# Optimization experiments

Measured on AMD Instinct MI355X. Metric: run time of the kernel, lower is better.

Reference implementation:

```python
import jax, jax.numpy as jnp
import numpy as np

# ---- CRF hyperparameters (init_kwargs) ----
NUM_CLASSES = 4
RADIUS = 10            # guided filter radius -> 21x21 kernel
EPS = 1e-4
THETA_GAMMA = 2.5
G_RADIUS = int(THETA_GAMMA * 4)  # gaussian layer radius = 10 -> 21x21 kernel
SPATIAL_COMPAT = 3.0
BILATERAL_COMPAT = 10.0
NUM_ITERATIONS = 5
RGB_W = np.array([0.2989, 0.5870, 0.1140], dtype=np.float32)  # tf rgb_to_grayscale


def _make_kernel(radius, theta):
    x, y = np.mgrid[-radius:radius + 1, -radius:radius + 1]
    k = np.exp(-(x ** 2 + y ** 2) / (2.0 * theta ** 2))
    k = k / k.sum()
    k[radius, radius] = 0.0  # zero out center (no self-message)
    return jnp.asarray(k, dtype=jnp.float32)

_GAUSS_K = _make_kernel(G_RADIUS, THETA_GAMMA)          # spatial gaussian kernel
_GUIDED_K = _make_kernel(RADIUS, RADIUS / 3.0)          # guided-filter gaussian kernel


def _depthwise(src, k2d, r):
    # src: [B,H,W,C], k2d: [kh,kw]; zero-padded depthwise conv (same as pad+VALID)
    c = src.shape[-1]
    kh, kw = k2d.shape
    k = jnp.broadcast_to(k2d[:, :, None, None], (kh, kw, 1, c))
    return jax.lax.conv_general_dilated(
        src, k, window_strides=(1, 1), padding=[(r, r), (r, r)],
        dimension_numbers=('NHWC', 'HWIO', 'NHWC'), feature_group_count=c)


def _gaussian(src):
    return _depthwise(src, _GAUSS_K, G_RADIUS)


def _guided(gray, p):
    # guided gaussian filter with single-channel guide `gray` [B,H,W,1]
    gf = lambda s: _depthwise(s, _GUIDED_K, RADIUS)
    mean_I = gf(gray)                       # [B,H,W,1]
    mean_p = gf(p)                          # [B,H,W,C]
    mean_Ip = gf(gray * p)
    cov_Ip = mean_Ip - mean_I * mean_p
    mean_II = gf(gray * gray)
    var_I = mean_II - mean_I * mean_I
    a = cov_Ip / (var_I + EPS)
    b = mean_p - a * mean_I
    return gf(a) * gray + gf(b)


def setup_inputs() -> dict:
    key = jax.random.key(0)
    k1, k2 = jax.random.split(key)
    unary = jax.random.normal(k1, (1, 512, 512, NUM_CLASSES), dtype=jnp.float32)
    image = jax.random.uniform(k2, (1, 512, 512, 3), dtype=jnp.float32)
    return {"unary": unary, "image": image}


def reference(unary, image):
    gray = (image @ jnp.asarray(RGB_W))[..., None]        # [B,H,W,1]
    ones = jnp.ones_like(unary)
    spatial_norm = _gaussian(ones)
    bilateral_norm = _guided(gray, ones)

    Q = jax.nn.softmax(-unary, axis=-1)
    for _ in range(NUM_ITERATIONS):
        spatial_out = _gaussian(Q) / spatial_norm
        bilateral_out = _guided(gray, Q) / bilateral_norm
        # spatial_weights = SPATIAL_COMPAT*I, bilateral_weights = BILATERAL_COMPAT*I,
        # compatibility = -I  => matmuls reduce to scalar scaling + negation
        message = SPATIAL_COMPAT * spatial_out + BILATERAL_COMPAT * bilateral_out
        pairwise = -message
        Q = jax.nn.softmax(-unary - pairwise, axis=-1)
    return Q
```

## Files before the change

kernel.cpp:

```cpp
#include <hip/hip_runtime.h>
#include <hip/hip_cooperative_groups.h>
#include <math.h>

namespace cg = cooperative_groups;

#define W 512
#define H 512
#define NPIX (W*H)
#define RAD 10
#define KS 21
#define CRF_EPS 1e-4f

#define TX 32
#define TY 8
#define CIN (TX + 2*RAD)
#define RIN (TY + 2*RAD)
#define GX (W / TX)
#define GY (H / TY)
#define NBLK (GX*GY)
#define NVT (CIN * 4)

#define SM_BYTES 29952
#define OFF_R1 23296

struct W21 { float w[KS]; };

struct Params {
    const float4* unary;
    const float*  image;
    float*  gray;
    float4* Q;
    float2* a1b1;
    float4* a_arr;
    float4* b_arr;
    float4* Qfinal;
    W21 wg, wu;
    float c0g, c0u;
};

__device__ __forceinline__ float4 f4(float x, float y, float z, float w_) {
    return make_float4(x, y, z, w_);
}
__device__ __forceinline__ float4 fma4(float s, float4 a, float4 acc) {
    acc.x = fmaf(s, a.x, acc.x); acc.y = fmaf(s, a.y, acc.y);
    acc.z = fmaf(s, a.z, acc.z); acc.w = fmaf(s, a.w, acc.w);
    return acc;
}
__device__ __forceinline__ int swz(int b, int N) {
    return (b & 7) * (N >> 3) + (b >> 3);
}


__global__ __launch_bounds__(256, 5) void k_crf(Params P) {
    cg::grid_group grid = cg::this_grid();
    __shared__ __align__(16) char smem[SM_BYTES];
    float4* sQ  = (float4*)smem;
    float2* s2t = (float2*)smem;
    float2* ii0 = (float2*)smem;
    float*  sG  = (float*)(smem + OFF_R1);
    float2* ii1 = (float2*)(smem + OFF_R1);
    float4* i0  = (float4*)smem;
    float4* i1  = (float4*)(smem + 6656);
    float4* i2  = (float4*)(smem + OFF_R1);
    float4* ia  = (float4*)(smem + OFF_R1);
    float4* ib  = (float4*)smem;

    int t = threadIdx.x;
    int L = swz(blockIdx.x, NBLK);
    int x0 = (L & (GX - 1)) * TX, y0 = (L >> 4) * TY;
    int row = t >> 5, col = t & 31;
    int py = y0 + row, px = x0 + col;
    int p = py * W + px;
    int vc = t % CIN, vr0 = (t / CIN) * 2;
    int cidx = (row + RAD) * CIN + col + RAD;

    {
        int pi = blockIdx.x * 256 + t;
        float r = P.image[3 * pi], g = P.image[3 * pi + 1], b = P.image[3 * pi + 2];
        P.gray[pi] = 0.2989f * r + 0.5870f * g + 0.1140f * b;
        float4 u0 = P.unary[pi];
        float mn = fminf(fminf(u0.x, u0.y), fminf(u0.z, u0.w));
        float ex = expf(mn - u0.x), ey = expf(mn - u0.y);
        float ez = expf(mn - u0.z), ew = expf(mn - u0.w);
        float inv = 1.f / (ex + ey + ez + ew);
        P.Q[pi] = f4(ex * inv, ey * inv, ez * inv, ew * inv);
    }
    float4 u = P.unary[p];
    float Sgx = 0.f, Sgy = 0.f, Sux = 0.f, Suy = 0.f;
    #pragma unroll
    for (int d = -RAD; d <= RAD; ++d) {
        int xx = px + d, yy = py + d;
        if (xx >= 0 && xx < W) { Sgx += P.wg.w[d + RAD]; Sux += P.wu.w[d + RAD]; }
        if (yy >= 0 && yy < H) { Sgy += P.wg.w[d + RAD]; Suy += P.wu.w[d + RAD]; }
    }
    float s3 = 3.f / (Sgx * Sgy - P.c0g);
    grid.sync();

    for (int i = t; i < RIN * CIN; i += 256) {
        int r = i / CIN, c = i - r * CIN;
        int gx = x0 + c - RAD, gy = y0 + r - RAD;
        float g = 0.f;
        if ((unsigned)gx < W && (unsigned)gy < H) g = P.gray[gy * W + gx];
        sG[i] = g;
    }
    __syncthreads();
    if (t < NVT) {
        float2 acc0 = make_float2(0.f, 0.f), acc1 = acc0;
        #pragma unroll
        for (int s = 0; s < 22; ++s) {
            float g = sG[(vr0 + s) * CIN + vc];
            if (s <= 20) { float wgv = P.wu.w[s] * g; acc0.x += wgv; acc0.y = fmaf(wgv, g, acc0.y); }
            if (s >= 1)  { float wgv = P.wu.w[s-1] * g; acc1.x += wgv; acc1.y = fmaf(wgv, g, acc1.y); }
        }
        ii0[vr0 * CIN + vc] = acc0;
        ii0[(vr0 + 1) * CIN + vc] = acc1;
    }
    __syncthreads();
    float gv = sG[cidx];
    float mI, iv, ibn;
    {
        float2 A = make_float2(0.f, 0.f);
        #pragma unroll
        for (int d = 0; d < KS; ++d) {
            float2 v = ii0[row * CIN + col + d];
            A.x = fmaf(P.wu.w[d], v.x, A.x);
            A.y = fmaf(P.wu.w[d], v.y, A.y);
        }
        mI = A.x - P.c0u * gv;
        float mII = A.y - P.c0u * gv * gv;
        iv = 1.f / ((mII - mI * mI) + CRF_EPS);
        float N = Sux * Suy - P.c0u;
        float a1v = mI * (1.f - N) * iv;
        float b1v = N - a1v * mI;
        P.a1b1[p] = make_float2(a1v, b1v);
    }
    grid.sync();

    for (int i = t; i < RIN * CIN; i += 256) {
        int r = i / CIN, c = i - r * CIN;
        int gx = x0 + c - RAD, gy = y0 + r - RAD;
        float2 v = make_float2(0.f, 0.f);
        if ((unsigned)gx < W && (unsigned)gy < H) v = P.a1b1[gy * W + gx];
        s2t[i] = v;
    }
    __syncthreads();
    if (t < NVT) {
        float2 acc0 = make_float2(0.f, 0.f), acc1 = acc0;
        #pragma unroll
        for (int s = 0; s < 22; ++s) {
            float2 v = s2t[(vr0 + s) * CIN + vc];
            if (s <= 20) { acc0.x = fmaf(P.wu.w[s], v.x, acc0.x); acc0.y = fmaf(P.wu.w[s], v.y, acc0.y); }
            if (s >= 1)  { acc1.x = fmaf(P.wu.w[s-1], v.x, acc1.x); acc1.y = fmaf(P.wu.w[s-1], v.y, acc1.y); }
        }
        ii1[vr0 * CIN + vc] = acc0;
        ii1[(vr0 + 1) * CIN + vc] = acc1;
    }
    __syncthreads();
    {
        float2 A = make_float2(0.f, 0.f);
        #pragma unroll
        for (int d = 0; d < KS; ++d) {
            float2 v = ii1[row * CIN + col + d];
            A.x = fmaf(P.wu.w[d], v.x, A.x);
            A.y = fmaf(P.wu.w[d], v.y, A.y);
        }
        float2 cen = s2t[cidx];
        float va = A.x - P.c0u * cen.x;
        float vb = A.y - P.c0u * cen.y;
        ibn = 10.f / (va * gv + vb);
    }

    float px_part, py_part, pz_part, pw_part;
    for (int it = 0; it < 5; ++it) {
        __syncthreads();
        for (int i = t; i < RIN * CIN; i += 256) {
            int r = i / CIN, c = i - r * CIN;
            int gx = x0 + c - RAD, gy = y0 + r - RAD;
            float4 q = f4(0.f, 0.f, 0.f, 0.f); float g = 0.f;
            if ((unsigned)gx < W && (unsigned)gy < H) {
                int pp = gy * W + gx; q = P.Q[pp]; g = P.gray[pp];
            }
            sQ[i] = q; sG[i] = g;
        }
        __syncthreads();
        float4 Qc = sQ[cidx];
        float4 a0[2], a1r[2], a2[2];
        if (t < NVT) {
            #pragma unroll
            for (int j = 0; j < 2; ++j) { a0[j] = f4(0,0,0,0); a1r[j] = a0[j]; a2[j] = a0[j]; }
            #pragma unroll
            for (int s = 0; s < 22; ++s) {
                float4 q = sQ[(vr0 + s) * CIN + vc];
                float g = sG[(vr0 + s) * CIN + vc];
                float4 gq = f4(g * q.x, g * q.y, g * q.z, g * q.w);
                if (s <= 20) {
                    a0[0]  = fma4(P.wg.w[s], q, a0[0]);
                    a1r[0] = fma4(P.wu.w[s], q, a1r[0]);
                    a2[0]  = fma4(P.wu.w[s], gq, a2[0]);
                }
                if (s >= 1) {
                    a0[1]  = fma4(P.wg.w[s-1], q, a0[1]);
                    a1r[1] = fma4(P.wu.w[s-1], q, a1r[1]);
                    a2[1]  = fma4(P.wu.w[s-1], gq, a2[1]);
                }
            }
        }
        __syncthreads();
        if (t < NVT) {
            #pragma unroll
            for (int j = 0; j < 2; ++j) {
                i0[(vr0 + j) * CIN + vc] = a0[j];
                i1[(vr0 + j) * CIN + vc] = a1r[j];
                i2[(vr0 + j) * CIN + vc] = a2[j];
            }
        }
        __syncthreads();
        {
            float4 A0 = f4(0,0,0,0), A1 = A0, A2 = A0;
            #pragma unroll
            for (int d = 0; d < KS; ++d) {
                A0 = fma4(P.wg.w[d], i0[row * CIN + col + d], A0);
                A1 = fma4(P.wu.w[d], i1[row * CIN + col + d], A1);
                A2 = fma4(P.wu.w[d], i2[row * CIN + col + d], A2);
            }
            float4 g4  = fma4(-P.c0g, Qc, A0);
            float4 m4  = fma4(-P.c0u, Qc, A1);
            float4 mi4 = fma4(-P.c0u * gv, Qc, A2);
            float4 a, b;
            a.x = (mi4.x - mI * m4.x) * iv; a.y = (mi4.y - mI * m4.y) * iv;
            a.z = (mi4.z - mI * m4.z) * iv; a.w = (mi4.w - mI * m4.w) * iv;
            b.x = m4.x - a.x * mI; b.y = m4.y - a.y * mI;
            b.z = m4.z - a.z * mI; b.w = m4.w - a.w * mI;
            px_part = fmaf(s3, g4.x, -u.x); py_part = fmaf(s3, g4.y, -u.y);
            pz_part = fmaf(s3, g4.z, -u.z); pw_part = fmaf(s3, g4.w, -u.w);
            P.a_arr[p] = a; P.b_arr[p] = b;
        }
        grid.sync();

        for (int i = t; i < RIN * CIN; i += 256) {
            int r = i / CIN, c = i - r * CIN;
            int gx = x0 + c - RAD, gy = y0 + r - RAD;
            float4 v = f4(0.f, 0.f, 0.f, 0.f);
            if ((unsigned)gx < W && (unsigned)gy < H) v = P.a_arr[gy * W + gx];
            sQ[i] = v;
        }
        __syncthreads();
        float4 Ac = sQ[cidx];
        if (t < NVT) {
            float4 va0 = f4(0,0,0,0), va1 = va0;
            #pragma unroll
            for (int s = 0; s < 22; ++s) {
                float4 v = sQ[(vr0 + s) * CIN + vc];
                if (s <= 20) va0 = fma4(P.wu.w[s], v, va0);
                if (s >= 1)  va1 = fma4(P.wu.w[s-1], v, va1);
            }
            ia[vr0 * CIN + vc] = va0;
            ia[(vr0 + 1) * CIN + vc] = va1;
        }
        __syncthreads();
        for (int i = t; i < RIN * CIN; i += 256) {
            int r = i / CIN, c = i - r * CIN;
            int gx = x0 + c - RAD, gy = y0 + r - RAD;
            float4 v = f4(0.f, 0.f, 0.f, 0.f);
            if ((unsigned)gx < W && (unsigned)gy < H) v = P.b_arr[gy * W + gx];
            sQ[i] = v;
        }
        __syncthreads();
        float4 Bc = sQ[cidx];
        float4 vb0 = f4(0,0,0,0), vb1 = vb0;
        if (t < NVT) {
            #pragma unroll
            for (int s = 0; s < 22; ++s) {
                float4 v = sQ[(vr0 + s) * CIN + vc];
                if (s <= 20) vb0 = fma4(P.wu.w[s], v, vb0);
                if (s >= 1)  vb1 = fma4(P.wu.w[s-1], v, vb1);
            }
        }
        __syncthreads();
        if (t < NVT) {
            ib[vr0 * CIN + vc] = vb0;
            ib[(vr0 + 1) * CIN + vc] = vb1;
        }
        __syncthreads();
        {
            float4 VA = f4(0,0,0,0), VB = VA;
            #pragma unroll
            for (int d = 0; d < KS; ++d) {
                VA = fma4(P.wu.w[d], ia[row * CIN + col + d], VA);
                VB = fma4(P.wu.w[d], ib[row * CIN + col + d], VB);
            }
            float4 a4 = fma4(-P.c0u, Ac, VA);
            float4 b4 = fma4(-P.c0u, Bc, VB);
            float lx = fmaf(fmaf(a4.x, gv, b4.x), ibn, px_part);
            float ly = fmaf(fmaf(a4.y, gv, b4.y), ibn, py_part);
            float lz = fmaf(fmaf(a4.z, gv, b4.z), ibn, pz_part);
            float lw = fmaf(fmaf(a4.w, gv, b4.w), ibn, pw_part);
            float m = fmaxf(fmaxf(lx, ly), fmaxf(lz, lw));
            float ex = expf(lx - m), ey = expf(ly - m);
            float ez = expf(lz - m), ew = expf(lw - m);
            float inv = 1.f / (ex + ey + ez + ew);
            float4 qn = f4(ex * inv, ey * inv, ez * inv, ew * inv);
            if (it == 4) P.Qfinal[p] = qn;
            else         P.Q[p] = qn;
        }
        if (it < 4) grid.sync();
    }
}


__global__ __launch_bounds__(256) void fb_init(const float* __restrict__ img,
        const float4* __restrict__ unary, float* __restrict__ gray,
        float4* __restrict__ Q, float* __restrict__ Sg, float* __restrict__ Su,
        W21 wg, W21 wu) {
    int t = threadIdx.x;
    if (blockIdx.x < 2) {
        int x = blockIdx.x * 256 + t;
        float sg = 0.f, su = 0.f;
        #pragma unroll
        for (int d = -RAD; d <= RAD; ++d) {
            int xx = x + d;
            if (xx >= 0 && xx < W) { sg += wg.w[d + RAD]; su += wu.w[d + RAD]; }
        }
        Sg[x] = sg; Su[x] = su;
    }
    int b = swz(blockIdx.x, NPIX / 256);
    int p = b * 256 + t;
    float r = img[3 * p], g = img[3 * p + 1], bch = img[3 * p + 2];
    gray[p] = 0.2989f * r + 0.5870f * g + 0.1140f * bch;
    float4 u = unary[p];
    float mn = fminf(fminf(u.x, u.y), fminf(u.z, u.w));
    float ex = expf(mn - u.x), ey = expf(mn - u.y), ez = expf(mn - u.z), ew = expf(mn - u.w);
    float inv = 1.f / (ex + ey + ez + ew);
    Q[p] = f4(ex * inv, ey * inv, ez * inv, ew * inv);
}

__global__ __launch_bounds__(256, 4) void fb_s1(const float* __restrict__ gray,
        const float* __restrict__ Su, float* __restrict__ mean_I,
        float* __restrict__ inv_var, float2* __restrict__ a1b1,
        W21 wu, float c0u) {
    __shared__ float  sg[RIN][CIN];
    __shared__ float2 ii[TY][CIN];
    int L = swz(blockIdx.x, NBLK);
    int x0 = (L & (GX - 1)) * TX, y0 = (L >> 4) * TY;
    int t = threadIdx.x;
    for (int i = t; i < RIN * CIN; i += 256) {
        int r = i / CIN, c = i - r * CIN;
        int gx = x0 + c - RAD, gy = y0 + r - RAD;
        float g = 0.f;
        if ((unsigned)gx < W && (unsigned)gy < H) g = gray[gy * W + gx];
        sg[r][c] = g;
    }
    __syncthreads();
    if (t < NVT) {
        int c = t % CIN, r0 = (t / CIN) * 2;
        float2 acc0 = make_float2(0.f, 0.f), acc1 = acc0;
        #pragma unroll
        for (int s = 0; s < 22; ++s) {
            float g = sg[r0 + s][c];
            if (s <= 20) { float wgv = wu.w[s] * g; acc0.x += wgv; acc0.y = fmaf(wgv, g, acc0.y); }
            if (s >= 1)  { float wgv = wu.w[s-1] * g; acc1.x += wgv; acc1.y = fmaf(wgv, g, acc1.y); }
        }
        ii[r0][c] = acc0; ii[r0 + 1][c] = acc1;
    }
    __syncthreads();
    int row = t >> 5, col = t & 31;
    float2 A = make_float2(0.f, 0.f);
    #pragma unroll
    for (int d = 0; d < KS; ++d) {
        float2 v = ii[row][col + d];
        A.x = fmaf(wu.w[d], v.x, A.x);
        A.y = fmaf(wu.w[d], v.y, A.y);
    }
    int py = y0 + row, px = x0 + col;
    int p = py * W + px;
    float gc = sg[row + RAD][col + RAD];
    float mI = A.x - c0u * gc;
    float mII = A.y - c0u * gc * gc;
    float iv = 1.f / ((mII - mI * mI) + CRF_EPS);
    float N = Su[px] * Su[py] - c0u;
    float av = mI * (1.f - N) * iv;
    float bv = N - av * mI;
    mean_I[p] = mI; inv_var[p] = iv; a1b1[p] = make_float2(av, bv);
}

__global__ __launch_bounds__(256, 4) void fb_s2(const float2* __restrict__ a1b1,
        const float* __restrict__ gray, float* __restrict__ inv_bn,
        W21 wu, float c0u) {
    __shared__ float2 s2[RIN][CIN];
    __shared__ float2 ii[TY][CIN];
    int L = swz(blockIdx.x, NBLK);
    int x0 = (L & (GX - 1)) * TX, y0 = (L >> 4) * TY;
    int t = threadIdx.x;
    for (int i = t; i < RIN * CIN; i += 256) {
        int r = i / CIN, c = i - r * CIN;
        int gx = x0 + c - RAD, gy = y0 + r - RAD;
        float2 v = make_float2(0.f, 0.f);
        if ((unsigned)gx < W && (unsigned)gy < H) v = a1b1[gy * W + gx];
        s2[r][c] = v;
    }
    __syncthreads();
    if (t < NVT) {
        int c = t % CIN, r0 = (t / CIN) * 2;
        float2 acc0 = make_float2(0.f, 0.f), acc1 = acc0;
        #pragma unroll
        for (int s = 0; s < 22; ++s) {
            float2 v = s2[r0 + s][c];
            if (s <= 20) { acc0.x = fmaf(wu.w[s], v.x, acc0.x); acc0.y = fmaf(wu.w[s], v.y, acc0.y); }
            if (s >= 1)  { acc1.x = fmaf(wu.w[s-1], v.x, acc1.x); acc1.y = fmaf(wu.w[s-1], v.y, acc1.y); }
        }
        ii[r0][c] = acc0; ii[r0 + 1][c] = acc1;
    }
    __syncthreads();
    int row = t >> 5, col = t & 31;
    float2 A = make_float2(0.f, 0.f);
    #pragma unroll
    for (int d = 0; d < KS; ++d) {
        float2 v = ii[row][col + d];
        A.x = fmaf(wu.w[d], v.x, A.x);
        A.y = fmaf(wu.w[d], v.y, A.y);
    }
    int p = (y0 + row) * W + x0 + col;
    float2 cen = s2[row + RAD][col + RAD];
    float va = A.x - c0u * cen.x;
    float vb = A.y - c0u * cen.y;
    inv_bn[p] = 1.f / (va * gray[p] + vb);
}

__global__ __launch_bounds__(256, 4) void fb_f1(const float4* __restrict__ Q,
        const float* __restrict__ gray, const float* __restrict__ mean_I,
        const float* __restrict__ inv_var, const float* __restrict__ Sg,
        const float4* __restrict__ unary, float4* __restrict__ a_out,
        float4* __restrict__ b_out, float4* __restrict__ partial,
        W21 wg, W21 wu, float c0g, float c0u) {
    __shared__ __align__(16) char smem[23296 + 5824 + 6656];
    float4* sQ = (float4*)smem;
    float*  sG = (float*)(smem + 23296);
    float4* i2 = (float4*)(smem + 23296 + 5824);
    float4* i0 = (float4*)smem;
    float4* i1 = (float4*)(smem + 6656);
    int L = swz(blockIdx.x, NBLK);
    int x0 = (L & (GX - 1)) * TX, y0 = (L >> 4) * TY;
    int t = threadIdx.x;
    for (int i = t; i < RIN * CIN; i += 256) {
        int r = i / CIN, c = i - r * CIN;
        int gx = x0 + c - RAD, gy = y0 + r - RAD;
        float4 q = f4(0.f, 0.f, 0.f, 0.f); float g = 0.f;
        if ((unsigned)gx < W && (unsigned)gy < H) {
            int p = gy * W + gx; q = Q[p]; g = gray[p];
        }
        sQ[i] = q; sG[i] = g;
    }
    __syncthreads();
    int row = t >> 5, col = t & 31;
    int py = y0 + row, px = x0 + col;
    int p = py * W + px;
    float mI = mean_I[p], iv = inv_var[p];
    float4 u = unary[p];
    float sgx = Sg[px], sgy = Sg[py];
    float4 Qc = sQ[(row + RAD) * CIN + col + RAD];
    float  gc = sG[(row + RAD) * CIN + col + RAD];
    float4 a0[2], a1[2], a2[2];
    int vc = t % CIN, vr0 = (t / CIN) * 2;
    if (t < NVT) {
        #pragma unroll
        for (int j = 0; j < 2; ++j) { a0[j] = f4(0,0,0,0); a1[j] = a0[j]; a2[j] = a0[j]; }
        #pragma unroll
        for (int s = 0; s < 22; ++s) {
            float4 q = sQ[(vr0 + s) * CIN + vc];
            float g = sG[(vr0 + s) * CIN + vc];
            float4 gq = f4(g * q.x, g * q.y, g * q.z, g * q.w);
            if (s <= 20) {
                a0[0] = fma4(wg.w[s], q, a0[0]);
                a1[0] = fma4(wu.w[s], q, a1[0]);
                a2[0] = fma4(wu.w[s], gq, a2[0]);
            }
            if (s >= 1) {
                a0[1] = fma4(wg.w[s-1], q, a0[1]);
                a1[1] = fma4(wu.w[s-1], q, a1[1]);
                a2[1] = fma4(wu.w[s-1], gq, a2[1]);
            }
        }
    }
    __syncthreads();
    if (t < NVT) {
        #pragma unroll
        for (int j = 0; j < 2; ++j) {
            i0[(vr0 + j) * CIN + vc] = a0[j];
            i1[(vr0 + j) * CIN + vc] = a1[j];
            i2[(vr0 + j) * CIN + vc] = a2[j];
        }
    }
    __syncthreads();
    float4 A0 = f4(0,0,0,0), A1 = A0, A2 = A0;
    #pragma unroll
    for (int d = 0; d < KS; ++d) {
        A0 = fma4(wg.w[d], i0[row * CIN + col + d], A0);
        A1 = fma4(wu.w[d], i1[row * CIN + col + d], A1);
        A2 = fma4(wu.w[d], i2[row * CIN + col + d], A2);
    }
    float4 g4  = fma4(-c0g, Qc, A0);
    float4 m4  = fma4(-c0u, Qc, A1);
    float4 mi4 = fma4(-c0u * gc, Qc, A2);
    float4 a, b;
    a.x = (mi4.x - mI * m4.x) * iv; a.y = (mi4.y - mI * m4.y) * iv;
    a.z = (mi4.z - mI * m4.z) * iv; a.w = (mi4.w - mI * m4.w) * iv;
    b.x = m4.x - a.x * mI; b.y = m4.y - a.y * mI;
    b.z = m4.z - a.z * mI; b.w = m4.w - a.w * mI;
    float s3 = 3.f / (sgx * sgy - c0g);
    float4 part = f4(fmaf(s3, g4.x, -u.x), fmaf(s3, g4.y, -u.y),
                     fmaf(s3, g4.z, -u.z), fmaf(s3, g4.w, -u.w));
    a_out[p] = a; b_out[p] = b; partial[p] = part;
}

__global__ __launch_bounds__(256, 4) void fb_f2(const float4* __restrict__ A,
        const float4* __restrict__ B, const float4* __restrict__ partial,
        const float* __restrict__ gray, const float* __restrict__ inv_bn,
        float4* __restrict__ Qout, W21 wu, float c0u) {
    __shared__ __align__(16) char smem[23296 + 6656];
    float4* sT = (float4*)smem;
    float4* ia = (float4*)(smem + 23296);
    float4* ib = (float4*)smem;
    int L = swz(blockIdx.x, NBLK);
    int x0 = (L & (GX - 1)) * TX, y0 = (L >> 4) * TY;
    int t = threadIdx.x;
    int row = t >> 5, col = t & 31;
    int py = y0 + row, px = x0 + col;
    int p = py * W + px;
    int vc = t % CIN, vr0 = (t / CIN) * 2;
    float gv = gray[p];
    float ibn = 10.f * inv_bn[p];
    float4 part = partial[p];
    for (int i = t; i < RIN * CIN; i += 256) {
        int r = i / CIN, c = i - r * CIN;
        int gx = x0 + c - RAD, gy = y0 + r - RAD;
        float4 v = f4(0.f, 0.f, 0.f, 0.f);
        if ((unsigned)gx < W && (unsigned)gy < H) v = A[gy * W + gx];
        sT[i] = v;
    }
    __syncthreads();
    float4 Ac = sT[(row + RAD) * CIN + col + RAD];
    float4 va0 = f4(0,0,0,0), va1 = va0;
    if (t < NVT) {
        #pragma unroll
        for (int s = 0; s < 22; ++s) {
            float4 v = sT[(vr0 + s) * CIN + vc];
            if (s <= 20) va0 = fma4(wu.w[s], v, va0);
            if (s >= 1)  va1 = fma4(wu.w[s-1], v, va1);
        }
        ia[vr0 * CIN + vc] = va0;
        ia[(vr0 + 1) * CIN + vc] = va1;
    }
    __syncthreads();
    for (int i = t; i < RIN * CIN; i += 256) {
        int r = i / CIN, c = i - r * CIN;
        int gx = x0 + c - RAD, gy = y0 + r - RAD;
        float4 v = f4(0.f, 0.f, 0.f, 0.f);
        if ((unsigned)gx < W && (unsigned)gy < H) v = B[gy * W + gx];
        sT[i] = v;
    }
    __syncthreads();
    float4 Bc = sT[(row + RAD) * CIN + col + RAD];
    float4 vb0 = f4(0,0,0,0), vb1 = vb0;
    if (t < NVT) {
        #pragma unroll
        for (int s = 0; s < 22; ++s) {
            float4 v = sT[(vr0 + s) * CIN + vc];
            if (s <= 20) vb0 = fma4(wu.w[s], v, vb0);
            if (s >= 1)  vb1 = fma4(wu.w[s-1], v, vb1);
        }
    }
    __syncthreads();
    if (t < NVT) {
        ib[vr0 * CIN + vc] = vb0;
        ib[(vr0 + 1) * CIN + vc] = vb1;
    }
    __syncthreads();
    float4 VA = f4(0,0,0,0), VB = VA;
    #pragma unroll
    for (int d = 0; d < KS; ++d) {
        VA = fma4(wu.w[d], ia[row * CIN + col + d], VA);
        VB = fma4(wu.w[d], ib[row * CIN + col + d], VB);
    }
    float4 a4 = fma4(-c0u, Ac, VA);
    float4 b4 = fma4(-c0u, Bc, VB);
    float lx = fmaf(fmaf(a4.x, gv, b4.x), ibn, part.x);
    float ly = fmaf(fmaf(a4.y, gv, b4.y), ibn, part.y);
    float lz = fmaf(fmaf(a4.z, gv, b4.z), ibn, part.z);
    float lw = fmaf(fmaf(a4.w, gv, b4.w), ibn, part.w);
    float m = fmaxf(fmaxf(lx, ly), fmaxf(lz, lw));
    float ex = expf(lx - m), ey = expf(ly - m), ez = expf(lz - m), ew = expf(lw - m);
    float inv = 1.f / (ex + ey + ez + ew);
    Qout[p] = f4(ex * inv, ey * inv, ez * inv, ew * inv);
}


static void make_w_host(double theta, W21* w, float* c0) {
    double tmp[KS], s = 0.0;
    for (int d = -RAD; d <= RAD; ++d) {
        double v = exp(-(double)(d * d) / (2.0 * theta * theta));
        tmp[d + RAD] = v; s += v;
    }
    for (int i = 0; i < KS; ++i) w->w[i] = (float)(tmp[i] / s);
    *c0 = (float)(1.0 / (s * s));
}

extern "C" void kernel_launch(void* const* d_in, const int* in_sizes, int n_in,
                              void* d_out, int out_size, void* d_ws, size_t ws_size,
                              hipStream_t stream) {
    const float4* unary = (const float4*)d_in[0];
    const float* image = (const float*)d_in[1];
    float* wsf = (float*)d_ws;

    float*  gray    = wsf;
    float*  mean_I  = wsf + 262144;
    float*  inv_var = wsf + 524288;
    float2* a1b1    = (float2*)(wsf + 786432);
    float*  inv_bn  = wsf + 1310720;
    float*  Sg      = wsf + 1572864;
    float*  Su      = wsf + 1573376;
    float4* Q       = (float4*)(wsf + 1573888);
    float4* partial = (float4*)(wsf + 2622464);
    float4* a_arr   = (float4*)(wsf + 3671040);
    float4* b_arr   = (float4*)(wsf + 4719616);

    W21 wg, wu; float c0g, c0u;
    make_w_host(2.5, &wg, &c0g);
    make_w_host(10.0 / 3.0, &wu, &c0u);

    int dev = 0;
    (void)hipGetDevice(&dev);
    int coop = 0, nCU = 0, blkPerCU = 0;
    (void)hipDeviceGetAttribute(&coop, hipDeviceAttributeCooperativeLaunch, dev);
    (void)hipDeviceGetAttribute(&nCU, hipDeviceAttributeMultiprocessorCount, dev);
    (void)hipOccupancyMaxActiveBlocksPerMultiprocessor(&blkPerCU,
            (const void*)k_crf, 256, 0);
    bool useCoop = (coop != 0) && ((long)blkPerCU * nCU >= NBLK);

    hipError_t st = hipErrorUnknown;
    if (useCoop) {
        Params P;
        P.unary = unary; P.image = image; P.gray = gray; P.Q = Q;
        P.a1b1 = a1b1; P.a_arr = a_arr; P.b_arr = b_arr;
        P.Qfinal = (float4*)d_out;
        P.wg = wg; P.wu = wu; P.c0g = c0g; P.c0u = c0u;
        void* args[] = { &P };
        st = hipLaunchCooperativeKernel((const void*)k_crf, dim3(NBLK), dim3(256),
                                        args, 0, stream);
    }
    if (st != hipSuccess) {
        dim3 bl(256), grEl(NPIX / 256), grT(NBLK);
        fb_init<<<grEl, bl, 0, stream>>>(image, unary, gray, Q, Sg, Su, wg, wu);
        fb_s1<<<grT, bl, 0, stream>>>(gray, Su, mean_I, inv_var, a1b1, wu, c0u);
        fb_s2<<<grT, bl, 0, stream>>>(a1b1, gray, inv_bn, wu, c0u);
        for (int it = 0; it < 5; ++it) {
            fb_f1<<<grT, bl, 0, stream>>>(Q, gray, mean_I, inv_var, Sg,
                                          unary, a_arr, b_arr, partial, wg, wu, c0g, c0u);
            float4* qdst = (it == 4) ? (float4*)d_out : Q;
            fb_f2<<<grT, bl, 0, stream>>>(a_arr, b_arr, partial, gray, inv_bn, qdst,
                                          wu, c0u);
        }
    }
}
```

Measured before the change: 170.7 us.

## Replace grid-wide barriers with neighbor-only flag synchronization

Swaps each cooperative grid.sync for per-block release flags plus acquire-spins on the 3x5 neighbourhood of tiles whose halos the block reads. The initial gray/softmax pass now writes the block's own pixels so only neighbours need to be ready. The aim is to remove the cost of full-device barriers and let blocks drift apart in time. The change adds a memset of the flag array per launch and relies on co-residency of all blocks for the spin-waits to make progress. It also risks write-after-read hazards when a fast block overwrites Q or a/b data that a lagging neighbour is still loading.

```diff
diff --git a/kernel.cpp b/kernel.cpp
--- a/kernel.cpp
+++ b/kernel.cpp
@@ -1,8 +1,5 @@
 #include <hip/hip_runtime.h>
-#include <hip/hip_cooperative_groups.h>
 #include <math.h>
-
-namespace cg = cooperative_groups;
 
 #define W 512
 #define H 512
@@ -22,6 +19,8 @@
 
 #define SM_BYTES 29952
 #define OFF_R1 23296
+
+#define FLAG_STRIDE 32
 
 struct W21 { float w[KS]; };
 
@@ -34,6 +33,7 @@
     float4* a_arr;
     float4* b_arr;
     float4* Qfinal;
+    unsigned* flags;
     W21 wg, wu;
     float c0g, c0u;
 };
@@ -51,8 +51,30 @@
 }
 
 
+__device__ __forceinline__ void publish(unsigned* flags, int L, unsigned v) {
+    __syncthreads();
+    if (threadIdx.x == 0)
+        __hip_atomic_store(flags + (size_t)L * FLAG_STRIDE, v,
+                           __ATOMIC_RELEASE, __HIP_MEMORY_SCOPE_AGENT);
+}
+
+__device__ __forceinline__ void waitnb(unsigned* flags, int bx, int by, unsigned v) {
+    int t = threadIdx.x;
+    if (t < 15) {
+        int dx = (t % 3) - 1, dy = (t / 3) - 2;
+        int nx = bx + dx, ny = by + dy;
+        if (((dx | dy) != 0) && (unsigned)nx < GX && (unsigned)ny < GY) {
+            unsigned* f = flags + (size_t)(ny * GX + nx) * FLAG_STRIDE;
+            while (__hip_atomic_load(f, __ATOMIC_ACQUIRE,
+                                     __HIP_MEMORY_SCOPE_AGENT) < v)
+                __builtin_amdgcn_s_sleep(4);
+        }
+    }
+    __syncthreads();
+}
+
+
 __global__ __launch_bounds__(256, 5) void k_crf(Params P) {
-    cg::grid_group grid = cg::this_grid();
     __shared__ __align__(16) char smem[SM_BYTES];
     float4* sQ  = (float4*)smem;
     float2* s2t = (float2*)smem;
@@ -67,25 +89,25 @@
 
     int t = threadIdx.x;
     int L = swz(blockIdx.x, NBLK);
-    int x0 = (L & (GX - 1)) * TX, y0 = (L >> 4) * TY;
+    int bx = L & (GX - 1), by = L >> 4;
+    int x0 = bx * TX, y0 = by * TY;
     int row = t >> 5, col = t & 31;
     int py = y0 + row, px = x0 + col;
     int p = py * W + px;
     int vc = t % CIN, vr0 = (t / CIN) * 2;
     int cidx = (row + RAD) * CIN + col + RAD;
-
+    unsigned* flags = P.flags;
+
+    float4 u = P.unary[p];
     {
-        int pi = blockIdx.x * 256 + t;
-        float r = P.image[3 * pi], g = P.image[3 * pi + 1], b = P.image[3 * pi + 2];
-        P.gray[pi] = 0.2989f * r + 0.5870f * g + 0.1140f * b;
-        float4 u0 = P.unary[pi];
-        float mn = fminf(fminf(u0.x, u0.y), fminf(u0.z, u0.w));
-        float ex = expf(mn - u0.x), ey = expf(mn - u0.y);
-        float ez = expf(mn - u0.z), ew = expf(mn - u0.w);
+        float r = P.image[3 * p], g = P.image[3 * p + 1], b = P.image[3 * p + 2];
+        P.gray[p] = 0.2989f * r + 0.5870f * g + 0.1140f * b;
+        float mn = fminf(fminf(u.x, u.y), fminf(u.z, u.w));
+        float ex = expf(mn - u.x), ey = expf(mn - u.y);
+        float ez = expf(mn - u.z), ew = expf(mn - u.w);
         float inv = 1.f / (ex + ey + ez + ew);
-        P.Q[pi] = f4(ex * inv, ey * inv, ez * inv, ew * inv);
-    }
-    float4 u = P.unary[p];
+        P.Q[p] = f4(ex * inv, ey * inv, ez * inv, ew * inv);
+    }
     float Sgx = 0.f, Sgy = 0.f, Sux = 0.f, Suy = 0.f;
     #pragma unroll
     for (int d = -RAD; d <= RAD; ++d) {
@@ -94,7 +116,8 @@
         if (yy >= 0 && yy < H) { Sgy += P.wg.w[d + RAD]; Suy += P.wu.w[d + RAD]; }
     }
     float s3 = 3.f / (Sgx * Sgy - P.c0g);
-    grid.sync();
+    publish(flags, L, 1);
+    waitnb(flags, bx, by, 1);
 
     for (int i = t; i < RIN * CIN; i += 256) {
         int r = i / CIN, c = i - r * CIN;
@@ -134,7 +157,8 @@
         float b1v = N - a1v * mI;
         P.a1b1[p] = make_float2(a1v, b1v);
     }
-    grid.sync();
+    publish(flags, L, 2);
+    waitnb(flags, bx, by, 2);
 
     for (int i = t; i < RIN * CIN; i += 256) {
         int r = i / CIN, c = i - r * CIN;
@@ -172,6 +196,7 @@
 
     float px_part, py_part, pz_part, pw_part;
     for (int it = 0; it < 5; ++it) {
+        if (it > 0) waitnb(flags, bx, by, 2 + 2 * it);
         __syncthreads();
         for (int i = t; i < RIN * CIN; i += 256) {
             int r = i / CIN, c = i - r * CIN;
@@ -235,7 +260,8 @@
             pz_part = fmaf(s3, g4.z, -u.z); pw_part = fmaf(s3, g4.w, -u.w);
             P.a_arr[p] = a; P.b_arr[p] = b;
         }
-        grid.sync();
+        publish(flags, L, 3 + 2 * it);
+        waitnb(flags, bx, by, 3 + 2 * it);
 
         for (int i = t; i < RIN * CIN; i += 256) {
             int r = i / CIN, c = i - r * CIN;
@@ -303,7 +329,7 @@
             if (it == 4) P.Qfinal[p] = qn;
             else         P.Q[p] = qn;
         }
-        if (it < 4) grid.sync();
+        if (it < 4) publish(flags, L, 4 + 2 * it);
     }
 }
 
@@ -622,6 +648,7 @@
     float4* partial = (float4*)(wsf + 2622464);
     float4* a_arr   = (float4*)(wsf + 3671040);
     float4* b_arr   = (float4*)(wsf + 4719616);
+    unsigned* flags = (unsigned*)(wsf + 262144);
 
     W21 wg, wu; float c0g, c0u;
     make_w_host(2.5, &wg, &c0g);
@@ -638,10 +665,12 @@
 
     hipError_t st = hipErrorUnknown;
     if (useCoop) {
+        (void)hipMemsetAsync(flags, 0, (size_t)NBLK * FLAG_STRIDE * sizeof(unsigned),
+                             stream);
         Params P;
         P.unary = unary; P.image = image; P.gray = gray; P.Q = Q;
         P.a1b1 = a1b1; P.a_arr = a_arr; P.b_arr = b_arr;
-        P.Qfinal = (float4*)d_out;
+        P.Qfinal = (float4*)d_out; P.flags = flags;
         P.wg = wg; P.wu = wu; P.c0g = c0g; P.c0u = c0u;
         void* args[] = { &P };
         st = hipLaunchCooperativeKernel((const void*)k_crf, dim3(NBLK), dim3(256),
```

Result: no change. 170.4 us (-0.2%).
